# Optimization experiments

Measured on AMD Instinct MI355X. Metric: run time of the kernel, lower is better.

The kernel has to match this reference:

```python
import jax, jax.numpy as jnp
import numpy as np
import math

LATENT = 64
COMP = 20
EM_ITERS = 5
GAMMA1 = 1.0  # 1/sqrt(gamma), gamma=1
LOG_NORM_C = -0.5 * math.log(2.0 * math.pi)


def setup_inputs() -> dict:
    key = jax.random.key(0)
    k1, k2, k3 = jax.random.split(key, 3)
    z = jax.random.normal(k1, (64, 8192, LATENT), dtype=jnp.float32)
    # small causal adjacency so (I - A) and the inverses are well conditioned
    A = jax.random.normal(k2, (LATENT, LATENT), dtype=jnp.float32) * 0.05
    init_idx = jax.random.randint(k3, (64, COMP), 0, 8192)
    return {"z": z, "A": A, "init_idx": init_idx}


def _em_step(X, pi, mean, trace, IA):
    # X: [B,N,L], pi/trace: [B,K], mean: [B,K,L], IA = I - A: [L,L]
    B, N, L = X.shape
    # gaussian_log_prob(X, mean) with logvar=0, summed over L, expanded as
    # -0.5*||x-m||^2 + L*c, computed without materializing a [B,N,K,L] tensor
    sq_x = jnp.sum(X * X, axis=-1)                      # [B,N]
    sq_m = jnp.sum(mean * mean, axis=-1)                # [B,K]
    cross = jnp.einsum('bnl,bkl->bnk', X, mean)         # [B,N,K]
    term_x = -0.5 * (sq_x[:, :, None] - 2.0 * cross + sq_m[:, None, :]) + L * LOG_NORM_C
    # gaussian_log_prob(causal(mean), 0, logvar=log(trace) broadcast over L)
    cm = jnp.einsum('bkl,lm->bkm', mean, IA)            # causal(mean)
    lt = jnp.log(trace)                                  # [B,K]
    term_c = -0.5 * (L * lt + jnp.sum(cm * cm, axis=-1) / trace) + L * LOG_NORM_C
    ll = term_x + jnp.log(pi)[:, None, :] + term_c[:, None, :]   # [B,N,K]
    post = jax.nn.softmax(ll, axis=-1)
    Nk = jnp.sum(post, axis=1)                           # [B,K]
    Nk = jnp.where(Nk == 0.0, jnp.asarray(1e-22, Nk.dtype), Nk)
    new_trace = GAMMA1 * jnp.ones_like(Nk)
    # std_causal = causal(I*trace) = trace*(I-A); trace is gamma1 for every
    # (b,k), so the [B,K,L,L] inverse collapses to one shared [L,L] inverse.
    I = jnp.eye(L, dtype=X.dtype)
    M = jnp.linalg.inv(I + (GAMMA1 ** 2) * (IA @ IA.T))
    new_pi = Nk / jnp.sum(Nk, axis=-1, keepdims=True)    # fix_pi=False
    new_mean = jnp.einsum('bnk,bnl->bkl', post, X) / Nk[:, :, None]
    new_mean = jnp.einsum('bkl,lm->bkm', new_mean, M)
    return new_pi, new_mean, new_trace


def reference(z, A, init_idx):
    # EM-based Gaussian-mixture prior (get_unsupervised_prior) of GMVAE
    B, N, L = z.shape
    I = jnp.eye(L, dtype=z.dtype)
    IA = I - A  # linear CausalEncoder: causal(x) = x @ (I - A)
    pi = jnp.full((B, COMP), 1.0 / COMP, dtype=z.dtype)
    trace = jnp.ones((B, COMP), dtype=z.dtype)
    # initial inverse: inv(I + (1/trace) * sig_cas @ sig_cas.T), trace == 1
    M0 = jnp.linalg.inv(I + IA @ IA.T)
    mean = jnp.take_along_axis(z, init_idx[:, :, None], axis=1)  # [B,K,L]
    mean = jnp.einsum('bkl,lm->bkm', mean, M0)
    for _ in range(EM_ITERS):
        pi, mean, trace = _em_step(z, pi, mean, trace, IA)
    return pi, mean, trace
```

## Files before the change

kernel.cpp:

```cpp
#include <hip/hip_runtime.h>
#include <math.h>

#define BB 64
#define NN 8192
#define LL 64
#define KK 20
#define TILE 128
#define NT 8
#define CHUNKS 8
#define ZSB 72
#define ZTS 140
#define PTTS 136
#define AS 132
#define TS 68

typedef float f32x4 __attribute__((ext_vector_type(4)));
typedef short s16x8 __attribute__((ext_vector_type(8)));
typedef short s16x4 __attribute__((ext_vector_type(4)));
typedef unsigned short u16x4 __attribute__((ext_vector_type(4)));
typedef unsigned short u16x2 __attribute__((ext_vector_type(2)));

#define MFMA_BF16 __builtin_amdgcn_mfma_f32_16x16x32_bf16

__device__ __forceinline__ unsigned short f2bf(float f) {
    unsigned int u = __float_as_uint(f);
    u += 0x7fffu + ((u >> 16) & 1u);
    return (unsigned short)(u >> 16);
}
__device__ __forceinline__ float bf2f(unsigned short h) {
    return __uint_as_float(((unsigned int)h) << 16);
}


__global__ __launch_bounds__(256) void k_setup(const float* __restrict__ A,
                                               float* __restrict__ IA,
                                               float* __restrict__ M) {
    __shared__ __align__(16) float iaT[64][TS];
    __shared__ __align__(16) float aug[64][AS];
    __shared__ __align__(16) float prow[AS];
    int t = threadIdx.x;
    for (int i = t; i < 4096; i += 256) {
        int r = i >> 6, c = i & 63;
        float v = (r == c ? 1.0f : 0.0f) - A[i];
        IA[i] = v;
        iaT[c][r] = v;
    }
    __syncthreads();
    {
        int r0 = (t >> 4) << 2;
        int c0 = (t & 15) << 2;
        float s[4][4];
        #pragma unroll
        for (int a = 0; a < 4; ++a)
            #pragma unroll
            for (int bq = 0; bq < 4; ++bq) s[a][bq] = 0.f;
        for (int l = 0; l < 64; ++l) {
            float4 u = *(const float4*)&iaT[l][r0];
            float4 v = *(const float4*)&iaT[l][c0];
            float uu[4] = {u.x, u.y, u.z, u.w};
            float vv[4] = {v.x, v.y, v.z, v.w};
            #pragma unroll
            for (int a = 0; a < 4; ++a)
                #pragma unroll
                for (int bq = 0; bq < 4; ++bq) s[a][bq] += uu[a] * vv[bq];
        }
        #pragma unroll
        for (int a = 0; a < 4; ++a) {
            int r = r0 + a;
            float4 w;
            w.x = s[a][0] + (r == c0 + 0 ? 1.f : 0.f);
            w.y = s[a][1] + (r == c0 + 1 ? 1.f : 0.f);
            w.z = s[a][2] + (r == c0 + 2 ? 1.f : 0.f);
            w.w = s[a][3] + (r == c0 + 3 ? 1.f : 0.f);
            *(float4*)&aug[r][c0] = w;
            float4 id;
            id.x = (r == c0 + 0 ? 1.f : 0.f);
            id.y = (r == c0 + 1 ? 1.f : 0.f);
            id.z = (r == c0 + 2 ? 1.f : 0.f);
            id.w = (r == c0 + 3 ? 1.f : 0.f);
            *(float4*)&aug[r][64 + c0] = id;
        }
    }
    __syncthreads();
    int r = t & 63;
    int cbase = (t >> 6) * 32;
    for (int k = 0; k < 64; ++k) {
        float pivinv = 1.0f / aug[k][k];
        float f = aug[r][k];
        if (r == k) {
            #pragma unroll
            for (int i = 0; i < 8; ++i) {
                float4 v = *(const float4*)&aug[k][cbase + 4 * i];
                v.x *= pivinv; v.y *= pivinv; v.z *= pivinv; v.w *= pivinv;
                *(float4*)&prow[cbase + 4 * i] = v;
            }
        }
        __syncthreads();
        if (r != k) {
            #pragma unroll
            for (int i = 0; i < 8; ++i) {
                float4 p = *(const float4*)&prow[cbase + 4 * i];
                float4 v = *(const float4*)&aug[r][cbase + 4 * i];
                v.x -= f * p.x; v.y -= f * p.y; v.z -= f * p.z; v.w -= f * p.w;
                *(float4*)&aug[r][cbase + 4 * i] = v;
            }
        } else {
            #pragma unroll
            for (int i = 0; i < 8; ++i)
                *(float4*)&aug[k][cbase + 4 * i] = *(const float4*)&prow[cbase + 4 * i];
        }
        __syncthreads();
    }
    for (int i = t; i < 4096; i += 256) {
        int rr = i >> 6, c = i & 63;
        M[i] = aug[rr][64 + c];
    }
}

__global__ __launch_bounds__(64) void k_init(const float* __restrict__ z,
                                             const int* __restrict__ idxs,
                                             const float* __restrict__ M,
                                             const float* __restrict__ IA,
                                             float* __restrict__ out_mean,
                                             float* __restrict__ bias,
                                             float* __restrict__ nk,
                                             float* __restrict__ macc) {
    int k = blockIdx.x, b = blockIdx.y;
    int l = threadIdx.x;
    int bk = b * KK + k;
    __shared__ float srow[64];
    __shared__ float smean[64];
    int idx = idxs[bk];
    srow[l] = z[((size_t)b * NN + idx) * LL + l];
    __syncthreads();
    float nm = 0.f;
    #pragma unroll 8
    for (int m = 0; m < 64; ++m) nm += srow[m] * M[m * 64 + l];
    out_mean[(size_t)bk * LL + l] = nm;
    smean[l] = nm;
    __syncthreads();
    float cm = 0.f;
    #pragma unroll 8
    for (int m = 0; m < 64; ++m) cm += smean[m] * IA[m * 64 + l];
    float sqm = nm * nm;
    float sqc = cm * cm;
    for (int off = 32; off > 0; off >>= 1) {
        sqm += __shfl_down(sqm, off);
        sqc += __shfl_down(sqc, off);
    }
    if (l == 0) {
        bias[bk] = logf(1.0f / KK) - 0.5f * (sqm + sqc);
        nk[bk] = 0.f;
    }
    macc[(size_t)bk * LL + l] = 0.f;
}

__global__ __launch_bounds__(256, 2) void k_empass(const float* __restrict__ z,
                                                   const float* __restrict__ mean,
                                                   const float* __restrict__ bias,
                                                   float* __restrict__ nk,
                                                   float* __restrict__ macc) {
    __shared__ __align__(16) unsigned short zhl[2][TILE][ZSB];
    __shared__ __align__(16) unsigned short mhl[2][32][ZSB];
    __shared__ __align__(16) unsigned short zT[64][ZTS];
    __shared__ __align__(16) unsigned short ptT[32][PTTS];
    __shared__ float bias_s[KK];
    __shared__ float nkred[4][KK];
    int t = threadIdx.x;
    int lane = t & 63;
    int q = t >> 6;
    int ln = lane & 15;
    int lg4 = lane >> 4;
    int s = t & 15;
    int b = blockIdx.y;
    size_t zbase = ((size_t)b * NN + (size_t)blockIdx.x * (TILE * NT)) * LL;

    for (int i = t; i < KK * LL; i += 256) {
        float f = mean[(size_t)b * KK * LL + i];
        int k = i >> 6, c = i & 63;
        unsigned short h = f2bf(f);
        mhl[0][k][c] = h;
        mhl[1][k][c] = f2bf(f - bf2f(h));
    }
    for (int i = 20 * ZSB + t; i < 32 * ZSB; i += 256) {
        (&mhl[0][0][0])[i] = 0;
        (&mhl[1][0][0])[i] = 0;
    }
    {
        unsigned int* pz = (unsigned int*)&ptT[20][0];
        for (int i = t; i < 6 * PTTS; i += 256) pz[i] = 0;
    }
    if (t < KK) bias_s[t] = bias[b * KK + t];
    __syncthreads();
    float bias0 = bias_s[ln];
    float bias1 = (ln < 4) ? bias_s[16 + ln] : 0.f;

    const float4* zg = (const float4*)(z + zbase);
    f32x4 bacc0 = {0.f, 0.f, 0.f, 0.f};
    f32x4 bacc1 = {0.f, 0.f, 0.f, 0.f};
    float nk0 = 0.f, nk1 = 0.f;

    for (int tt = 0; tt < NT; ++tt) {
        if (tt > 0) __syncthreads();
        #pragma unroll
        for (int u = 0; u < 4; ++u) {
            int r0 = u * 32 + ((t >> 4) << 1);
            float4 v0 = zg[tt * 2048 + r0 * 16 + s];
            float4 v1 = zg[tt * 2048 + (r0 + 1) * 16 + s];
            unsigned short h0 = f2bf(v0.x), h1 = f2bf(v0.y), h2 = f2bf(v0.z), h3 = f2bf(v0.w);
            unsigned short g0 = f2bf(v1.x), g1 = f2bf(v1.y), g2 = f2bf(v1.z), g3 = f2bf(v1.w);
            *(u16x4*)&zhl[0][r0][4 * s]     = (u16x4){h0, h1, h2, h3};
            *(u16x4*)&zhl[0][r0 + 1][4 * s] = (u16x4){g0, g1, g2, g3};
            *(u16x4*)&zhl[1][r0][4 * s]     = (u16x4){f2bf(v0.x - bf2f(h0)), f2bf(v0.y - bf2f(h1)),
                                                      f2bf(v0.z - bf2f(h2)), f2bf(v0.w - bf2f(h3))};
            *(u16x4*)&zhl[1][r0 + 1][4 * s] = (u16x4){f2bf(v1.x - bf2f(g0)), f2bf(v1.y - bf2f(g1)),
                                                      f2bf(v1.z - bf2f(g2)), f2bf(v1.w - bf2f(g3))};
            *(u16x2*)&zT[4 * s + 0][r0] = (u16x2){h0, g0};
            *(u16x2*)&zT[4 * s + 1][r0] = (u16x2){h1, g1};
            *(u16x2*)&zT[4 * s + 2][r0] = (u16x2){h2, g2};
            *(u16x2*)&zT[4 * s + 3][r0] = (u16x2){h3, g3};
        }
        __syncthreads();

        f32x4 acc[2][2];
        #pragma unroll
        for (int rt = 0; rt < 2; ++rt) {
            acc[rt][0] = (f32x4){bias0, bias0, bias0, bias0};
            acc[rt][1] = (f32x4){bias1, bias1, bias1, bias1};
        }
        #pragma unroll
        for (int ks = 0; ks < 2; ++ks) {
            int kc = ks * 32 + lg4 * 8;
            s16x8 bh0 = *(const s16x8*)&mhl[0][ln][kc];
            s16x8 bl0 = *(const s16x8*)&mhl[1][ln][kc];
            s16x8 bh1 = *(const s16x8*)&mhl[0][16 + ln][kc];
            s16x8 bl1 = *(const s16x8*)&mhl[1][16 + ln][kc];
            #pragma unroll
            for (int rt = 0; rt < 2; ++rt) {
                int arow = q * 32 + rt * 16 + ln;
                s16x8 ah = *(const s16x8*)&zhl[0][arow][kc];
                s16x8 al = *(const s16x8*)&zhl[1][arow][kc];
                acc[rt][0] = MFMA_BF16(ah, bh0, acc[rt][0], 0, 0, 0);
                acc[rt][0] = MFMA_BF16(ah, bl0, acc[rt][0], 0, 0, 0);
                acc[rt][0] = MFMA_BF16(al, bh0, acc[rt][0], 0, 0, 0);
                acc[rt][1] = MFMA_BF16(ah, bh1, acc[rt][1], 0, 0, 0);
                acc[rt][1] = MFMA_BF16(ah, bl1, acc[rt][1], 0, 0, 0);
                acc[rt][1] = MFMA_BF16(al, bh1, acc[rt][1], 0, 0, 0);
            }
        }
        #pragma unroll
        for (int rt = 0; rt < 2; ++rt) {
            #pragma unroll
            for (int rg = 0; rg < 4; ++rg) {
                float v0 = acc[rt][0][rg];
                float v1 = (ln < 4) ? acc[rt][1][rg] : -INFINITY;
                float m = fmaxf(v0, v1);
                m = fmaxf(m, __shfl_xor(m, 1));
                m = fmaxf(m, __shfl_xor(m, 2));
                m = fmaxf(m, __shfl_xor(m, 4));
                m = fmaxf(m, __shfl_xor(m, 8));
                float e0 = __expf(v0 - m);
                float e1 = (ln < 4) ? __expf(v1 - m) : 0.f;
                float sm = e0 + e1;
                sm += __shfl_xor(sm, 1);
                sm += __shfl_xor(sm, 2);
                sm += __shfl_xor(sm, 4);
                sm += __shfl_xor(sm, 8);
                float inv = 1.0f / sm;
                float p0 = e0 * inv;
                float p1 = e1 * inv;
                nk0 += p0;
                nk1 += p1;
                int row = q * 32 + rt * 16 + lg4 * 4 + rg;
                ptT[ln][row] = f2bf(p0);
                if (ln < 4) ptT[16 + ln][row] = f2bf(p1);
            }
        }
        __syncthreads();

        #pragma unroll
        for (int ch = 0; ch < 4; ++ch) {
            int rr = ch * 32 + lg4 * 8;
            s16x4 zb0 = *(const s16x4*)&zT[q * 16 + ln][rr];
            s16x4 zb1 = *(const s16x4*)&zT[q * 16 + ln][rr + 4];
            s16x8 bfr = (s16x8){zb0[0], zb0[1], zb0[2], zb0[3], zb1[0], zb1[1], zb1[2], zb1[3]};
            s16x8 af0 = *(const s16x8*)&ptT[ln][rr];
            s16x8 af1 = *(const s16x8*)&ptT[16 + ln][rr];
            bacc0 = MFMA_BF16(af0, bfr, bacc0, 0, 0, 0);
            bacc1 = MFMA_BF16(af1, bfr, bacc1, 0, 0, 0);
        }
    }

    nk0 += __shfl_xor(nk0, 16);
    nk0 += __shfl_xor(nk0, 32);
    nk1 += __shfl_xor(nk1, 16);
    nk1 += __shfl_xor(nk1, 32);
    if (lane < 16) nkred[q][lane] = nk0;
    if (lane < 4) nkred[q][16 + lane] = nk1;

    int col = q * 16 + ln;
    #pragma unroll
    for (int reg = 0; reg < 4; ++reg) {
        int comp = lg4 * 4 + reg;
        atomicAdd(&macc[((size_t)b * KK + comp) * LL + col], bacc0[reg]);
    }
    if (lg4 == 0) {
        #pragma unroll
        for (int reg = 0; reg < 4; ++reg)
            atomicAdd(&macc[((size_t)b * KK + 16 + reg) * LL + col], bacc1[reg]);
    }
    __syncthreads();
    if (t < KK) {
        float sum = nkred[0][t] + nkred[1][t] + nkred[2][t] + nkred[3][t];
        atomicAdd(&nk[b * KK + t], sum);
    }
}

__global__ __launch_bounds__(64) void k_final(const float* __restrict__ Mm,
                                              const float* __restrict__ IA,
                                              float* __restrict__ nk,
                                              float* __restrict__ macc,
                                              float* __restrict__ bias,
                                              float* __restrict__ out_pi,
                                              float* __restrict__ out_mean,
                                              float* __restrict__ out_trace) {
    int k = blockIdx.x, b = blockIdx.y;
    int l = threadIdx.x;
    int bk = b * KK + k;
    __shared__ float sraw[64];
    __shared__ float smean[64];
    float Nk = nk[bk];
    if (Nk == 0.f) Nk = 1e-22f;
    float pi = Nk / (float)NN;
    float raw = macc[(size_t)bk * LL + l] / Nk;
    sraw[l] = raw;
    __syncthreads();
    float nm = 0.f;
    #pragma unroll 8
    for (int m = 0; m < 64; ++m) nm += sraw[m] * Mm[m * 64 + l];
    out_mean[(size_t)bk * LL + l] = nm;
    smean[l] = nm;
    __syncthreads();
    float cm = 0.f;
    #pragma unroll 8
    for (int m = 0; m < 64; ++m) cm += smean[m] * IA[m * 64 + l];
    float sqm = nm * nm;
    float sqc = cm * cm;
    for (int off = 32; off > 0; off >>= 1) {
        sqm += __shfl_down(sqm, off);
        sqc += __shfl_down(sqc, off);
    }
    if (l == 0) {
        bias[bk] = logf(pi) - 0.5f * (sqm + sqc);
        out_pi[bk] = pi;
        out_trace[bk] = 1.0f;
        nk[bk] = 0.f;
    }
    macc[(size_t)bk * LL + l] = 0.f;
}

extern "C" void kernel_launch(void* const* d_in, const int* in_sizes, int n_in,
                              void* d_out, int out_size, void* d_ws, size_t ws_size,
                              hipStream_t stream) {
    const float* z = (const float*)d_in[0];
    const float* A = (const float*)d_in[1];
    const int* idxs = (const int*)d_in[2];

    float* out_pi = (float*)d_out;
    float* out_mean = out_pi + BB * KK;
    float* out_trace = out_mean + (size_t)BB * KK * LL;

    float* ws = (float*)d_ws;
    float* IA = ws;
    float* M = ws + 4096;
    float* bias = ws + 8192;
    float* nk = ws + 9472;
    float* macc = ws + 10752;

    k_setup<<<1, 256, 0, stream>>>(A, IA, M);
    k_init<<<dim3(KK, BB), 64, 0, stream>>>(z, idxs, M, IA, out_mean, bias, nk, macc);
    for (int it = 0; it < 5; ++it) {
        k_empass<<<dim3(CHUNKS, BB), 256, 0, stream>>>(z, out_mean, bias, nk, macc);
        k_final<<<dim3(KK, BB), 64, 0, stream>>>(M, IA, nk, macc, bias, out_pi, out_mean, out_trace);
    }
}
```

Before: 350.4 us.

## Fuse finalize into EM pass via last-block counter, transpose MFMA, pipeline pivot

Drops the separate k_final launch: the last workgroup per batch, detected with a threadfence plus atomic counter, does the mean/bias update with atomicExch readback of the accumulators. The logit MFMA operands are swapped so each lane holds four components of one row, which shortens the softmax shuffle reductions and the Nk accumulation. The setup Gauss-Jordan step now builds the next pivot row during the current elimination, removing one barrier per step. This saves five launches and a round of shuffles, but serializes the finalize onto a single block per batch and relies on correct cross-block fence ordering.

Result: slower. 377.3 us (+7.7%).

```diff
diff --git a/kernel.cpp b/kernel.cpp
--- a/kernel.cpp
+++ b/kernel.cpp
@@ -37,7 +37,7 @@
                                                float* __restrict__ M) {
     __shared__ __align__(16) float iaT[64][TS];
     __shared__ __align__(16) float aug[64][AS];
-    __shared__ __align__(16) float prow[AS];
+    __shared__ __align__(16) float prowbuf[2][AS];
     int t = threadIdx.x;
     for (int i = t; i < 4096; i += 256) {
         int r = i >> 6, c = i & 63;
@@ -82,32 +82,45 @@
         }
     }
     __syncthreads();
-    int r = t & 63;
-    int cbase = (t >> 6) * 32;
+    int r = t >> 2;
+    int cbase = (t & 3) * 32;
+    if (r == 0) {
+        float pivinv = 1.0f / aug[0][0];
+        #pragma unroll
+        for (int i = 0; i < 8; ++i) {
+            float4 v = *(const float4*)&aug[0][cbase + 4 * i];
+            v.x *= pivinv; v.y *= pivinv; v.z *= pivinv; v.w *= pivinv;
+            *(float4*)&prowbuf[0][cbase + 4 * i] = v;
+        }
+    }
+    __syncthreads();
     for (int k = 0; k < 64; ++k) {
-        float pivinv = 1.0f / aug[k][k];
-        float f = aug[r][k];
+        const float* prow = prowbuf[k & 1];
+        float* prown = prowbuf[(k + 1) & 1];
         if (r == k) {
             #pragma unroll
-            for (int i = 0; i < 8; ++i) {
-                float4 v = *(const float4*)&aug[k][cbase + 4 * i];
-                v.x *= pivinv; v.y *= pivinv; v.z *= pivinv; v.w *= pivinv;
-                *(float4*)&prow[cbase + 4 * i] = v;
-            }
-        }
-        __syncthreads();
-        if (r != k) {
+            for (int i = 0; i < 8; ++i)
+                *(float4*)&aug[r][cbase + 4 * i] = *(const float4*)&prow[cbase + 4 * i];
+        } else {
+            float f = aug[r][k];
+            float4 v[8];
             #pragma unroll
             for (int i = 0; i < 8; ++i) {
                 float4 p = *(const float4*)&prow[cbase + 4 * i];
-                float4 v = *(const float4*)&aug[r][cbase + 4 * i];
-                v.x -= f * p.x; v.y -= f * p.y; v.z -= f * p.z; v.w -= f * p.w;
-                *(float4*)&aug[r][cbase + 4 * i] = v;
-            }
-        } else {
-            #pragma unroll
-            for (int i = 0; i < 8; ++i)
-                *(float4*)&aug[k][cbase + 4 * i] = *(const float4*)&prow[cbase + 4 * i];
+                float4 a = *(const float4*)&aug[r][cbase + 4 * i];
+                a.x -= f * p.x; a.y -= f * p.y; a.z -= f * p.z; a.w -= f * p.w;
+                *(float4*)&aug[r][cbase + 4 * i] = a;
+                v[i] = a;
+            }
+            if (r == k + 1) {
+                float pivinv = 1.0f / aug[k + 1][k + 1];
+                #pragma unroll
+                for (int i = 0; i < 8; ++i) {
+                    float4 w = v[i];
+                    w.x *= pivinv; w.y *= pivinv; w.z *= pivinv; w.w *= pivinv;
+                    *(float4*)&prown[cbase + 4 * i] = w;
+                }
+            }
         }
         __syncthreads();
     }
@@ -124,7 +137,8 @@
                                              float* __restrict__ out_mean,
                                              float* __restrict__ bias,
                                              float* __restrict__ nk,
-                                             float* __restrict__ macc) {
+                                             float* __restrict__ macc,
+                                             int* __restrict__ cnt) {
     int k = blockIdx.x, b = blockIdx.y;
     int l = threadIdx.x;
     int bk = b * KK + k;
@@ -151,21 +165,28 @@
     if (l == 0) {
         bias[bk] = logf(1.0f / KK) - 0.5f * (sqm + sqc);
         nk[bk] = 0.f;
+        if (k == 0) cnt[b] = 0;
     }
     macc[(size_t)bk * LL + l] = 0.f;
 }
 
 __global__ __launch_bounds__(256, 2) void k_empass(const float* __restrict__ z,
-                                                   const float* __restrict__ mean,
-                                                   const float* __restrict__ bias,
+                                                   float* __restrict__ mean,
+                                                   float* __restrict__ bias,
                                                    float* __restrict__ nk,
-                                                   float* __restrict__ macc) {
+                                                   float* __restrict__ macc,
+                                                   int* __restrict__ cnt,
+                                                   const float* __restrict__ M,
+                                                   const float* __restrict__ IA,
+                                                   float* __restrict__ out_pi,
+                                                   float* __restrict__ out_trace) {
     __shared__ __align__(16) unsigned short zhl[2][TILE][ZSB];
     __shared__ __align__(16) unsigned short mhl[2][32][ZSB];
     __shared__ __align__(16) unsigned short zT[64][ZTS];
     __shared__ __align__(16) unsigned short ptT[32][PTTS];
-    __shared__ float bias_s[KK];
+    __shared__ __align__(16) float bias_s[32];
     __shared__ float nkred[4][KK];
+    __shared__ int isLast;
     int t = threadIdx.x;
     int lane = t & 63;
     int q = t >> 6;
@@ -190,15 +211,16 @@
         unsigned int* pz = (unsigned int*)&ptT[20][0];
         for (int i = t; i < 6 * PTTS; i += 256) pz[i] = 0;
     }
-    if (t < KK) bias_s[t] = bias[b * KK + t];
-    __syncthreads();
-    float bias0 = bias_s[ln];
-    float bias1 = (ln < 4) ? bias_s[16 + ln] : 0.f;
+    if (t < 32) bias_s[t] = (t < KK) ? bias[b * KK + t] : -1e30f;
+    __syncthreads();
+    float4 b0 = *(const float4*)&bias_s[lg4 * 4];
+    float4 b1 = *(const float4*)&bias_s[16 + lg4 * 4];
 
     const float4* zg = (const float4*)(z + zbase);
     f32x4 bacc0 = {0.f, 0.f, 0.f, 0.f};
     f32x4 bacc1 = {0.f, 0.f, 0.f, 0.f};
-    float nk0 = 0.f, nk1 = 0.f;
+    float nkp0[4] = {0.f, 0.f, 0.f, 0.f};
+    float nkp1[4] = {0.f, 0.f, 0.f, 0.f};
 
     for (int tt = 0; tt < NT; ++tt) {
         if (tt > 0) __syncthreads();
@@ -222,58 +244,62 @@
         }
         __syncthreads();
 
-        f32x4 acc[2][2];
+        f32x4 acc0[2], acc1[2];
         #pragma unroll
         for (int rt = 0; rt < 2; ++rt) {
-            acc[rt][0] = (f32x4){bias0, bias0, bias0, bias0};
-            acc[rt][1] = (f32x4){bias1, bias1, bias1, bias1};
+            acc0[rt] = (f32x4){b0.x, b0.y, b0.z, b0.w};
+            acc1[rt] = (f32x4){b1.x, b1.y, b1.z, b1.w};
         }
         #pragma unroll
         for (int ks = 0; ks < 2; ++ks) {
             int kc = ks * 32 + lg4 * 8;
-            s16x8 bh0 = *(const s16x8*)&mhl[0][ln][kc];
-            s16x8 bl0 = *(const s16x8*)&mhl[1][ln][kc];
-            s16x8 bh1 = *(const s16x8*)&mhl[0][16 + ln][kc];
-            s16x8 bl1 = *(const s16x8*)&mhl[1][16 + ln][kc];
+            s16x8 mh0 = *(const s16x8*)&mhl[0][ln][kc];
+            s16x8 ml0 = *(const s16x8*)&mhl[1][ln][kc];
+            s16x8 mh1 = *(const s16x8*)&mhl[0][16 + ln][kc];
+            s16x8 ml1 = *(const s16x8*)&mhl[1][16 + ln][kc];
             #pragma unroll
             for (int rt = 0; rt < 2; ++rt) {
-                int arow = q * 32 + rt * 16 + ln;
-                s16x8 ah = *(const s16x8*)&zhl[0][arow][kc];
-                s16x8 al = *(const s16x8*)&zhl[1][arow][kc];
-                acc[rt][0] = MFMA_BF16(ah, bh0, acc[rt][0], 0, 0, 0);
-                acc[rt][0] = MFMA_BF16(ah, bl0, acc[rt][0], 0, 0, 0);
-                acc[rt][0] = MFMA_BF16(al, bh0, acc[rt][0], 0, 0, 0);
-                acc[rt][1] = MFMA_BF16(ah, bh1, acc[rt][1], 0, 0, 0);
-                acc[rt][1] = MFMA_BF16(ah, bl1, acc[rt][1], 0, 0, 0);
-                acc[rt][1] = MFMA_BF16(al, bh1, acc[rt][1], 0, 0, 0);
+                int zrow = q * 32 + rt * 16 + ln;
+                s16x8 zh = *(const s16x8*)&zhl[0][zrow][kc];
+                s16x8 zl = *(const s16x8*)&zhl[1][zrow][kc];
+                acc0[rt] = MFMA_BF16(mh0, zh, acc0[rt], 0, 0, 0);
+                acc0[rt] = MFMA_BF16(ml0, zh, acc0[rt], 0, 0, 0);
+                acc0[rt] = MFMA_BF16(mh0, zl, acc0[rt], 0, 0, 0);
+                acc1[rt] = MFMA_BF16(mh1, zh, acc1[rt], 0, 0, 0);
+                acc1[rt] = MFMA_BF16(ml1, zh, acc1[rt], 0, 0, 0);
+                acc1[rt] = MFMA_BF16(mh1, zl, acc1[rt], 0, 0, 0);
             }
         }
         #pragma unroll
         for (int rt = 0; rt < 2; ++rt) {
-            #pragma unroll
-            for (int rg = 0; rg < 4; ++rg) {
-                float v0 = acc[rt][0][rg];
-                float v1 = (ln < 4) ? acc[rt][1][rg] : -INFINITY;
-                float m = fmaxf(v0, v1);
-                m = fmaxf(m, __shfl_xor(m, 1));
-                m = fmaxf(m, __shfl_xor(m, 2));
-                m = fmaxf(m, __shfl_xor(m, 4));
-                m = fmaxf(m, __shfl_xor(m, 8));
-                float e0 = __expf(v0 - m);
-                float e1 = (ln < 4) ? __expf(v1 - m) : 0.f;
-                float sm = e0 + e1;
-                sm += __shfl_xor(sm, 1);
-                sm += __shfl_xor(sm, 2);
-                sm += __shfl_xor(sm, 4);
-                sm += __shfl_xor(sm, 8);
-                float inv = 1.0f / sm;
-                float p0 = e0 * inv;
-                float p1 = e1 * inv;
-                nk0 += p0;
-                nk1 += p1;
-                int row = q * 32 + rt * 16 + lg4 * 4 + rg;
-                ptT[ln][row] = f2bf(p0);
-                if (ln < 4) ptT[16 + ln][row] = f2bf(p1);
+            int zrow = q * 32 + rt * 16 + ln;
+            float m = fmaxf(fmaxf(fmaxf(acc0[rt][0], acc0[rt][1]), fmaxf(acc0[rt][2], acc0[rt][3])),
+                            fmaxf(fmaxf(acc1[rt][0], acc1[rt][1]), fmaxf(acc1[rt][2], acc1[rt][3])));
+            m = fmaxf(m, __shfl_xor(m, 16));
+            m = fmaxf(m, __shfl_xor(m, 32));
+            float e0[4], e1[4];
+            float sm = 0.f;
+            #pragma unroll
+            for (int j = 0; j < 4; ++j) {
+                e0[j] = __expf(acc0[rt][j] - m); sm += e0[j];
+                e1[j] = __expf(acc1[rt][j] - m); sm += e1[j];
+            }
+            sm += __shfl_xor(sm, 16);
+            sm += __shfl_xor(sm, 32);
+            float inv = 1.0f / sm;
+            #pragma unroll
+            for (int j = 0; j < 4; ++j) {
+                float p = e0[j] * inv;
+                nkp0[j] += p;
+                ptT[lg4 * 4 + j][zrow] = f2bf(p);
+            }
+            if (lg4 == 0) {
+                #pragma unroll
+                for (int j = 0; j < 4; ++j) {
+                    float p = e1[j] * inv;
+                    nkp1[j] += p;
+                    ptT[16 + j][zrow] = f2bf(p);
+                }
             }
         }
         __syncthreads();
@@ -291,12 +317,30 @@
         }
     }
 
-    nk0 += __shfl_xor(nk0, 16);
-    nk0 += __shfl_xor(nk0, 32);
-    nk1 += __shfl_xor(nk1, 16);
-    nk1 += __shfl_xor(nk1, 32);
-    if (lane < 16) nkred[q][lane] = nk0;
-    if (lane < 4) nkred[q][16 + lane] = nk1;
+    #pragma unroll
+    for (int j = 0; j < 4; ++j) {
+        nkp0[j] += __shfl_xor(nkp0[j], 1);
+        nkp0[j] += __shfl_xor(nkp0[j], 2);
+        nkp0[j] += __shfl_xor(nkp0[j], 4);
+        nkp0[j] += __shfl_xor(nkp0[j], 8);
+    }
+    if (ln == 0) {
+        #pragma unroll
+        for (int j = 0; j < 4; ++j) nkred[q][lg4 * 4 + j] = nkp0[j];
+    }
+    if (lg4 == 0) {
+        #pragma unroll
+        for (int j = 0; j < 4; ++j) {
+            nkp1[j] += __shfl_xor(nkp1[j], 1);
+            nkp1[j] += __shfl_xor(nkp1[j], 2);
+            nkp1[j] += __shfl_xor(nkp1[j], 4);
+            nkp1[j] += __shfl_xor(nkp1[j], 8);
+        }
+        if (ln == 0) {
+            #pragma unroll
+            for (int j = 0; j < 4; ++j) nkred[q][16 + j] = nkp1[j];
+        }
+    }
 
     int col = q * 16 + ln;
     #pragma unroll
@@ -314,49 +358,53 @@
         float sum = nkred[0][t] + nkred[1][t] + nkred[2][t] + nkred[3][t];
         atomicAdd(&nk[b * KK + t], sum);
     }
-}
-
-__global__ __launch_bounds__(64) void k_final(const float* __restrict__ Mm,
-                                              const float* __restrict__ IA,
-                                              float* __restrict__ nk,
-                                              float* __restrict__ macc,
-                                              float* __restrict__ bias,
-                                              float* __restrict__ out_pi,
-                                              float* __restrict__ out_mean,
-                                              float* __restrict__ out_trace) {
-    int k = blockIdx.x, b = blockIdx.y;
-    int l = threadIdx.x;
-    int bk = b * KK + k;
-    __shared__ float sraw[64];
-    __shared__ float smean[64];
-    float Nk = nk[bk];
-    if (Nk == 0.f) Nk = 1e-22f;
-    float pi = Nk / (float)NN;
-    float raw = macc[(size_t)bk * LL + l] / Nk;
-    sraw[l] = raw;
-    __syncthreads();
-    float nm = 0.f;
-    #pragma unroll 8
-    for (int m = 0; m < 64; ++m) nm += sraw[m] * Mm[m * 64 + l];
-    out_mean[(size_t)bk * LL + l] = nm;
-    smean[l] = nm;
-    __syncthreads();
-    float cm = 0.f;
-    #pragma unroll 8
-    for (int m = 0; m < 64; ++m) cm += smean[m] * IA[m * 64 + l];
-    float sqm = nm * nm;
-    float sqc = cm * cm;
-    for (int off = 32; off > 0; off >>= 1) {
-        sqm += __shfl_down(sqm, off);
-        sqc += __shfl_down(sqc, off);
-    }
-    if (l == 0) {
-        bias[bk] = logf(pi) - 0.5f * (sqm + sqc);
-        out_pi[bk] = pi;
-        out_trace[bk] = 1.0f;
-        nk[bk] = 0.f;
-    }
-    macc[(size_t)bk * LL + l] = 0.f;
+    __syncthreads();
+    if (t == 0) {
+        __threadfence();
+        int old = atomicAdd(&cnt[b], 1);
+        isLast = (old == CHUNKS - 1) ? 1 : 0;
+    }
+    __syncthreads();
+    if (!isLast) return;
+
+    float* fs = (float*)&zhl[0][0][0];
+    float* sraw = fs + q * 160;
+    float* smean = sraw + 64;
+    int l = lane;
+    #pragma unroll
+    for (int kc5 = 0; kc5 < 5; ++kc5) {
+        int comp = kc5 * 4 + q;
+        int bk = b * KK + comp;
+        size_t mb = (size_t)bk * LL;
+        float nkv = 0.f;
+        if (l == 0) nkv = atomicExch(&nk[bk], 0.f);
+        nkv = __shfl(nkv, 0);
+        float nkc = fmaxf(nkv, 1e-22f);
+        float raw = atomicExch(&macc[mb + l], 0.f) / nkc;
+        sraw[l] = raw;
+        float nm = 0.f;
+        #pragma unroll 8
+        for (int m = 0; m < 64; ++m) nm += sraw[m] * M[m * 64 + l];
+        mean[mb + l] = nm;
+        smean[l] = nm;
+        float cm = 0.f;
+        #pragma unroll 8
+        for (int m = 0; m < 64; ++m) cm += smean[m] * IA[m * 64 + l];
+        float sqm = nm * nm;
+        float sqc = cm * cm;
+        #pragma unroll
+        for (int off = 32; off > 0; off >>= 1) {
+            sqm += __shfl_down(sqm, off);
+            sqc += __shfl_down(sqc, off);
+        }
+        if (l == 0) {
+            float pi = nkc * (1.0f / NN);
+            bias[bk] = logf(pi) - 0.5f * (sqm + sqc);
+            out_pi[bk] = pi;
+            out_trace[bk] = 1.0f;
+        }
+    }
+    if (t == 0) cnt[b] = 0;
 }
 
 extern "C" void kernel_launch(void* const* d_in, const int* in_sizes, int n_in,
@@ -376,11 +424,12 @@
     float* bias = ws + 8192;
     float* nk = ws + 9472;
     float* macc = ws + 10752;
+    int* cnt = (int*)(ws + 92672);
 
     k_setup<<<1, 256, 0, stream>>>(A, IA, M);
-    k_init<<<dim3(KK, BB), 64, 0, stream>>>(z, idxs, M, IA, out_mean, bias, nk, macc);
+    k_init<<<dim3(KK, BB), 64, 0, stream>>>(z, idxs, M, IA, out_mean, bias, nk, macc, cnt);
     for (int it = 0; it < 5; ++it) {
-        k_empass<<<dim3(CHUNKS, BB), 256, 0, stream>>>(z, out_mean, bias, nk, macc);
-        k_final<<<dim3(KK, BB), 64, 0, stream>>>(M, IA, nk, macc, bias, out_pi, out_mean, out_trace);
-    }
-}
+        k_empass<<<dim3(CHUNKS, BB), 256, 0, stream>>>(z, out_mean, bias, nk, macc,
+                                                       cnt, M, IA, out_pi, out_trace);
+    }
+}
```
